# Kernel optimization log

Hardware: AMD Instinct MI355X
Metric: run time of the kernel (lower is better)

The kernel has to match this reference:

```python
import jax, jax.numpy as jnp
import numpy as np

BETA = 0.25


def setup_inputs() -> dict:
    key = jax.random.key(0)
    k1, k2, k3, k4 = jax.random.split(key, 4)
    e_dim, n_e = 512, 8192
    z = jax.random.normal(k1, (16, e_dim, 32, 32), dtype=jnp.float32)
    # nn.init.normal_(embedding.weight, std=e_dim**-0.5)
    emb_weight = jax.random.normal(k2, (n_e, e_dim), dtype=jnp.float32) * (e_dim ** -0.5)
    # torch Linear default init ~ U(-1/sqrt(in), 1/sqrt(in))
    lim = 1.0 / np.sqrt(e_dim)
    proj_w = jax.random.uniform(k3, (e_dim, e_dim), minval=-lim, maxval=lim, dtype=jnp.float32)
    proj_b = jax.random.uniform(k4, (e_dim,), minval=-lim, maxval=lim, dtype=jnp.float32)
    return {"z": z, "emb_weight": emb_weight, "proj_w": proj_w, "proj_b": proj_b}


def reference(z, emb_weight, proj_w, proj_b):
    # z: [B, C, H, W] -> [B, H, W, C]
    zc = jnp.transpose(z, (0, 2, 3, 1))
    B, H, W, C = zc.shape
    z_flat = zc.reshape(-1, C)                               # [N, C]
    # projected codebook: Linear(e_dim, e_dim) -> x @ W^T + b
    qc = emb_weight @ proj_w.T + proj_b                      # [n_e, C]
    # squared distances: ||z||^2 + ||qc||^2 - 2 z.qc
    d = (jnp.sum(z_flat ** 2, axis=1, keepdims=True)
         + jnp.sum(qc ** 2, axis=1)
         - 2.0 * jnp.einsum('nd,kd->nk', z_flat, qc))        # [N, n_e]
    idx = jnp.argmin(d, axis=1)                              # [N]
    z_q = qc[idx].reshape(zc.shape)                          # [B, H, W, C]
    # legacy=False commit loss
    commit_loss = (BETA * jnp.mean((jax.lax.stop_gradient(z_q) - zc) ** 2)
                   + jnp.mean((z_q - jax.lax.stop_gradient(zc)) ** 2))
    # straight-through
    z_q = zc + jax.lax.stop_gradient(z_q - zc)
    z_q = jnp.transpose(z_q, (0, 3, 1, 2))                   # [B, C, H, W]
    min_encoding_indices = idx.reshape(B, H, W)              # sane_index_shape=True
    return z_q, commit_loss, min_encoding_indices
```

## Files before the change

kernel.cpp:

```cpp
#include <hip/hip_runtime.h>

typedef unsigned int uint;
typedef unsigned short ushort;
typedef unsigned long long ulong64;
typedef __attribute__((ext_vector_type(8))) short short8;
typedef __attribute__((ext_vector_type(4))) float f32x4;

#define B_   16
#define C_   512
#define HW_  1024
#define N_   16384
#define K_   8192
#define EPS_ 0.25f

#define QC_OFF    0u
#define QC_SZ     (K_ * C_)
#define QN_OFF    (QC_OFF + QC_SZ)
#define QN_SZ     K_
#define ZN_OFF    (QN_OFF + QN_SZ)
#define ZN_SZ     N_
#define ZF_OFF    (ZN_OFF + ZN_SZ)
#define ZF_SZ     (N_ * C_)
#define ZH_OFF    (ZF_OFF + ZF_SZ)
#define ZH_SZ     (N_ * C_ / 2)
#define QH_OFF    (ZH_OFF + ZH_SZ)
#define QH_SZ     (K_ * C_ / 2)
#define WT_OFF    (QH_OFF + QH_SZ)
#define WT_SZ     (64 * N_ * 4)
#define IDXF_OFF  (WT_OFF + WT_SZ)
#define IDXF_SZ   N_
#define LOSS_OFF  (IDXF_OFF + IDXF_SZ)

#define OUT_ZQ    0
#define OUT_LOSS  8388608
#define OUT_IDX   8388609

__device__ __forceinline__ ushort f2bf(float f) {
    uint x = __float_as_uint(f);
    uint r = x + 0x7fffu + ((x >> 16) & 1u);
    return (ushort)(r >> 16);
}

__global__ __launch_bounds__(256) void transpose_z(const float* __restrict__ z,
                                                   float* __restrict__ zf,
                                                   ushort* __restrict__ zh) {
    __shared__ float ld[64][65];
    const int t = threadIdx.x;
    const int mt = blockIdx.x, ct = blockIdx.y, b = blockIdx.z;
    {
        const int cl = t >> 4, m4 = (t & 15) * 4;
#pragma unroll
        for (int cc = 0; cc < 4; ++cc) {
            const int c = ct * 64 + cc * 16 + cl;
            float4 v = *(const float4*)&z[((size_t)(b * 512 + c)) * 1024 + mt * 64 + m4];
            ld[cc * 16 + cl][m4 + 0] = v.x; ld[cc * 16 + cl][m4 + 1] = v.y;
            ld[cc * 16 + cl][m4 + 2] = v.z; ld[cc * 16 + cl][m4 + 3] = v.w;
        }
    }
    __syncthreads();
    {
        const int nl = t >> 4, c4 = (t & 15) * 4;
#pragma unroll
        for (int nn = 0; nn < 4; ++nn) {
            const int n_local = nn * 16 + nl;
            const size_t n = (size_t)b * 1024 + mt * 64 + n_local;
            float4 w;
            w.x = ld[c4 + 0][n_local]; w.y = ld[c4 + 1][n_local];
            w.z = ld[c4 + 2][n_local]; w.w = ld[c4 + 3][n_local];
            *(float4*)&zf[n * 512 + ct * 64 + c4] = w;
            ushort4 h; h.x = f2bf(w.x); h.y = f2bf(w.y); h.z = f2bf(w.z); h.w = f2bf(w.w);
            *(ushort4*)&zh[n * 512 + ct * 64 + c4] = h;
        }
    }
}

__global__ __launch_bounds__(256) void qc_gemm(const float* __restrict__ emb,
                                               const float* __restrict__ W,
                                               const float* __restrict__ bias,
                                               float* __restrict__ qc,
                                               ushort* __restrict__ qh) {
    __shared__ float As[16][132];
    __shared__ float Bs[16][68];
    const int t    = threadIdx.x;
    const int k0   = blockIdx.x * 128;
    const int c0   = blockIdx.y * 64;
    const int ty   = t >> 4, tx = t & 15;
    const int rowA = t >> 1;
    const int dqA  = (t & 1) * 8;
    const int rowB = t >> 2;
    const int dqB  = (t & 3) * 4;

    const float* pa = emb + (size_t)(k0 + rowA) * 512 + dqA;
    const float* pb = W   + (size_t)(c0 + rowB) * 512 + dqB;
    float4 ra0 = *(const float4*)&pa[0];
    float4 ra1 = *(const float4*)&pa[4];
    float4 rb  = *(const float4*)&pb[0];

    float acc[2][4][4] = {};
    for (int d0 = 0; d0 < 512; d0 += 16) {
        __syncthreads();
        As[dqA + 0][rowA] = ra0.x; As[dqA + 1][rowA] = ra0.y;
        As[dqA + 2][rowA] = ra0.z; As[dqA + 3][rowA] = ra0.w;
        As[dqA + 4][rowA] = ra1.x; As[dqA + 5][rowA] = ra1.y;
        As[dqA + 6][rowA] = ra1.z; As[dqA + 7][rowA] = ra1.w;
        Bs[dqB + 0][rowB] = rb.x;  Bs[dqB + 1][rowB] = rb.y;
        Bs[dqB + 2][rowB] = rb.z;  Bs[dqB + 3][rowB] = rb.w;
        if (d0 + 16 < 512) {
            ra0 = *(const float4*)&pa[d0 + 16];
            ra1 = *(const float4*)&pa[d0 + 20];
            rb  = *(const float4*)&pb[d0 + 16];
        }
        __syncthreads();
#pragma unroll
        for (int dd = 0; dd < 16; ++dd) {
            float4 a0 = *(const float4*)&As[dd][ty * 4];
            float4 a1 = *(const float4*)&As[dd][64 + ty * 4];
            float4 b0 = *(const float4*)&Bs[dd][tx * 4];
            float aa[2][4] = {{a0.x, a0.y, a0.z, a0.w}, {a1.x, a1.y, a1.z, a1.w}};
            float bb[4] = {b0.x, b0.y, b0.z, b0.w};
#pragma unroll
            for (int ih = 0; ih < 2; ++ih)
#pragma unroll
                for (int i = 0; i < 4; ++i)
#pragma unroll
                    for (int j = 0; j < 4; ++j)
                        acc[ih][i][j] += aa[ih][i] * bb[j];
        }
    }
#pragma unroll
    for (int ih = 0; ih < 2; ++ih)
#pragma unroll
        for (int i = 0; i < 4; ++i) {
            const size_t kr = (size_t)(k0 + ih * 64 + ty * 4 + i) * 512;
            const int cb = c0 + tx * 4;
            float4 v;
            v.x = acc[ih][i][0] + bias[cb + 0];
            v.y = acc[ih][i][1] + bias[cb + 1];
            v.z = acc[ih][i][2] + bias[cb + 2];
            v.w = acc[ih][i][3] + bias[cb + 3];
            *(float4*)&qc[kr + cb] = v;
            ushort4 h; h.x = f2bf(v.x); h.y = f2bf(v.y); h.z = f2bf(v.z); h.w = f2bf(v.w);
            *(ushort4*)&qh[kr + cb] = h;
        }
}

__global__ __launch_bounds__(256) void znorm_pairwise(const float* __restrict__ z,
                                                      float* __restrict__ zn) {
#pragma clang fp contract(off)
    const int n = blockIdx.x * 256 + threadIdx.x;
    const int b = n >> 10, m = n & 1023;
    const float* base = z + (size_t)b * C_ * HW_ + m;
    float s128[4];
#pragma unroll
    for (int blk = 0; blk < 4; ++blk) {
        float r[8];
#pragma unroll
        for (int j = 0; j < 8; ++j) {
            float v = base[(size_t)(blk * 128 + j) * HW_];
            r[j] = v * v;
        }
#pragma unroll 1
        for (int i = 8; i < 128; i += 8) {
#pragma unroll
            for (int j = 0; j < 8; ++j) {
                float v = base[(size_t)(blk * 128 + i + j) * HW_];
                float sq = v * v;
                r[j] = r[j] + sq;
            }
        }
        s128[blk] = ((r[0] + r[1]) + (r[2] + r[3])) + ((r[4] + r[5]) + (r[6] + r[7]));
    }
    zn[n] = (s128[0] + s128[1]) + (s128[2] + s128[3]);
}

__global__ __launch_bounds__(256) void qnorm_grouped(const float* __restrict__ qc,
                                                     float* __restrict__ qn) {
#pragma clang fp contract(off)
    const int t   = threadIdx.x;
    const int grp = t >> 3;
    const int j   = t & 7;
    const int k   = blockIdx.x * 32 + grp;
    const float* row = qc + (size_t)k * C_;
    float s[4];
#pragma unroll
    for (int blk = 0; blk < 4; ++blk) {
        float v0 = row[blk * 128 + j];
        float r  = v0 * v0;
#pragma unroll 1
        for (int i = 1; i < 16; ++i) {
            float v  = row[blk * 128 + i * 8 + j];
            float sq = v * v;
            r = r + sq;
        }
        float t1 = r  + __shfl_xor(r, 1, 64);
        float t2 = t1 + __shfl_xor(t1, 2, 64);
        float t3 = t2 + __shfl_xor(t2, 4, 64);
        s[blk] = t3;
    }
    if (j == 0) qn[k] = (s[0] + s[1]) + (s[2] + s[3]);
}

#define PH_BAR()   __builtin_amdgcn_s_barrier()
#define PH_LGKM()  asm volatile("s_waitcnt lgkmcnt(0)" ::: "memory")
#define PH_LGKM8() asm volatile("s_waitcnt lgkmcnt(8)" ::: "memory")
#define PH_VM4()   asm volatile("s_waitcnt vmcnt(4)" ::: "memory")

__device__ __forceinline__ short8 ld8(const short* p, int off) {
    return *(const short8*)(p + off);
}

__global__ __launch_bounds__(512, 2) void phaseA(const ushort* __restrict__ qh,
                                                 const ushort* __restrict__ zh,
                                                 const float* __restrict__ qn,
                                                 float* __restrict__ wtop) {
    __shared__ short lq[32768];
    __shared__ short lz[32768];
    const int t    = threadIdx.x;
    const int lane = t & 63;
    const int wv   = t >> 6;
    const int wk   = wv >> 2;
    const int wn   = wv & 3;
    const int n0   = blockIdx.x * 256;
    const int k0   = blockIdx.y * 256;

    const int l15 = lane & 15;
    const int hi8 = (lane >> 4) << 3;
    const int xr  = (l15 & 7) << 3;
    const short* pA0 = lq + wk * 8192 + l15 * 64 + ((hi8) ^ xr);
    const short* pA1 = lq + wk * 8192 + l15 * 64 + ((32 + hi8) ^ xr);
    const short* pB0 = lz + (wn >> 1) * 8192 + (wn & 1) * 4096 + l15 * 64 + ((hi8) ^ xr);
    const short* pB1 = lz + (wn >> 1) * 8192 + (wn & 1) * 4096 + l15 * 64 + ((32 + hi8) ^ xr);

    const int ch0 = t,        row0 = ch0 >> 3;
    const int ch1 = t + 512,  row1 = ch1 >> 3;
    const int ce0 = ((ch0 ^ row0) & 7) << 3;
    const int ce1 = ((ch1 ^ row1) & 7) << 3;
    const ushort* qsrc0 = qh + (size_t)(k0 + row0) * 512 + ce0;
    const ushort* qsrc1 = qh + (size_t)(k0 + row1) * 512 + ce1;
    const ushort* zsrc0 = zh + (size_t)(n0 + row0) * 512 + ce0;
    const ushort* zsrc1 = zh + (size_t)(n0 + row1) * 512 + ce1;
    short* qdst0 = lq + ch0 * 8;
    short* qdst1 = lq + ch1 * 8;
    short* zdst0 = lz + ch0 * 8;
    short* zdst1 = lz + ch1 * 8;

    auto stage_half = [&](int b, int h, int chunk) {
        const int co = chunk * 64;
        if (h < 2) {
            __builtin_amdgcn_global_load_lds(
                (const __attribute__((address_space(1))) uint*)(qsrc0 + h * 65536 + co),
                (__attribute__((address_space(3))) uint*)(qdst0 + (b * 2 + h) * 8192), 16, 0, 0);
            __builtin_amdgcn_global_load_lds(
                (const __attribute__((address_space(1))) uint*)(qsrc1 + h * 65536 + co),
                (__attribute__((address_space(3))) uint*)(qdst1 + (b * 2 + h) * 8192), 16, 0, 0);
        } else {
            __builtin_amdgcn_global_load_lds(
                (const __attribute__((address_space(1))) uint*)(zsrc0 + (h - 2) * 65536 + co),
                (__attribute__((address_space(3))) uint*)(zdst0 + (b * 2 + (h - 2)) * 8192), 16, 0, 0);
            __builtin_amdgcn_global_load_lds(
                (const __attribute__((address_space(1))) uint*)(zsrc1 + (h - 2) * 65536 + co),
                (__attribute__((address_space(3))) uint*)(zdst1 + (b * 2 + (h - 2)) * 8192), 16, 0, 0);
        }
    };

    f32x4 acc[8][4];
#pragma unroll
    for (int i = 0; i < 8; ++i)
#pragma unroll
        for (int j = 0; j < 4; ++j) acc[i][j] = (f32x4){0.f, 0.f, 0.f, 0.f};

    stage_half(0, 0, 0); stage_half(0, 1, 0); stage_half(0, 2, 0); stage_half(0, 3, 0);
    stage_half(1, 0, 1); stage_half(1, 1, 1);
    PH_VM4();
    PH_BAR();

    short8 a0[2][4], a1[2][4], b0[2][2], b1[2][2];

#pragma unroll 1
    for (int I = 0; I < 4; ++I) {
        const int tE = 2 * I;
        const int tO = 2 * I + 1;

#pragma unroll
        for (int i = 0; i < 4; ++i) {
            a0[0][i] = ld8(pA0, i * 1024);        a0[1][i] = ld8(pA1, i * 1024);
            a1[0][i] = ld8(pA0, 4096 + i * 1024); a1[1][i] = ld8(pA1, 4096 + i * 1024);
        }
#pragma unroll
        for (int jj = 0; jj < 2; ++jj) { b0[0][jj] = ld8(pB0, jj * 1024); b0[1][jj] = ld8(pB1, jj * 1024); }
        stage_half(1, 2, (tO) & 7); stage_half(1, 3, (tO) & 7);
        PH_LGKM8();
        PH_BAR(); PH_LGKM();
        __builtin_amdgcn_s_setprio(1);
#pragma unroll
        for (int kk = 0; kk < 2; ++kk)
#pragma unroll
            for (int i = 0; i < 4; ++i)
#pragma unroll
                for (int jj = 0; jj < 2; ++jj) {
                    acc[i][jj]     = __builtin_amdgcn_mfma_f32_16x16x32_bf16(a0[kk][i], b0[kk][jj], acc[i][jj], 0, 0, 0);
                    acc[4 + i][jj] = __builtin_amdgcn_mfma_f32_16x16x32_bf16(a1[kk][i], b0[kk][jj], acc[4 + i][jj], 0, 0, 0);
                }
        __builtin_amdgcn_s_setprio(0);
        PH_BAR();
#pragma unroll
        for (int jj = 0; jj < 2; ++jj) { b1[0][jj] = ld8(pB0, 2048 + jj * 1024); b1[1][jj] = ld8(pB1, 2048 + jj * 1024); }
        stage_half(0, 0, (tE + 2) & 7); stage_half(0, 1, (tE + 2) & 7);
        PH_BAR(); PH_LGKM();
        __builtin_amdgcn_s_setprio(1);
#pragma unroll
        for (int kk = 0; kk < 2; ++kk)
#pragma unroll
            for (int i = 0; i < 4; ++i)
#pragma unroll
                for (int jj = 0; jj < 2; ++jj) {
                    acc[i][2 + jj]     = __builtin_amdgcn_mfma_f32_16x16x32_bf16(a0[kk][i], b1[kk][jj], acc[i][2 + jj], 0, 0, 0);
                    acc[4 + i][2 + jj] = __builtin_amdgcn_mfma_f32_16x16x32_bf16(a1[kk][i], b1[kk][jj], acc[4 + i][2 + jj], 0, 0, 0);
                }
        __builtin_amdgcn_s_setprio(0);
        PH_VM4();
        PH_BAR();

#pragma unroll
        for (int i = 0; i < 4; ++i) {
            a0[0][i] = ld8(pA0, 16384 + i * 1024);        a0[1][i] = ld8(pA1, 16384 + i * 1024);
            a1[0][i] = ld8(pA0, 16384 + 4096 + i * 1024); a1[1][i] = ld8(pA1, 16384 + 4096 + i * 1024);
        }
#pragma unroll
        for (int jj = 0; jj < 2; ++jj) { b0[0][jj] = ld8(pB0, 16384 + jj * 1024); b0[1][jj] = ld8(pB1, 16384 + jj * 1024); }
        stage_half(0, 2, (tO + 1) & 7); stage_half(0, 3, (tO + 1) & 7);
        PH_LGKM8();
        PH_BAR(); PH_LGKM();
        __builtin_amdgcn_s_setprio(1);
#pragma unroll
        for (int kk = 0; kk < 2; ++kk)
#pragma unroll
            for (int i = 0; i < 4; ++i)
#pragma unroll
                for (int jj = 0; jj < 2; ++jj) {
                    acc[i][jj]     = __builtin_amdgcn_mfma_f32_16x16x32_bf16(a0[kk][i], b0[kk][jj], acc[i][jj], 0, 0, 0);
                    acc[4 + i][jj] = __builtin_amdgcn_mfma_f32_16x16x32_bf16(a1[kk][i], b0[kk][jj], acc[4 + i][jj], 0, 0, 0);
                }
        __builtin_amdgcn_s_setprio(0);
        PH_BAR();
#pragma unroll
        for (int jj = 0; jj < 2; ++jj) { b1[0][jj] = ld8(pB0, 16384 + 2048 + jj * 1024); b1[1][jj] = ld8(pB1, 16384 + 2048 + jj * 1024); }
        stage_half(1, 0, (tO + 2) & 7); stage_half(1, 1, (tO + 2) & 7);
        PH_BAR(); PH_LGKM();
        __builtin_amdgcn_s_setprio(1);
#pragma unroll
        for (int kk = 0; kk < 2; ++kk)
#pragma unroll
            for (int i = 0; i < 4; ++i)
#pragma unroll
                for (int jj = 0; jj < 2; ++jj) {
                    acc[i][2 + jj]     = __builtin_amdgcn_mfma_f32_16x16x32_bf16(a0[kk][i], b1[kk][jj], acc[i][2 + jj], 0, 0, 0);
                    acc[4 + i][2 + jj] = __builtin_amdgcn_mfma_f32_16x16x32_bf16(a1[kk][i], b1[kk][jj], acc[4 + i][2 + jj], 0, 0, 0);
                }
        __builtin_amdgcn_s_setprio(0);
        PH_VM4();
        PH_BAR();
    }

    const int q4 = (lane >> 4) * 4;
    float v1[4], v2[4];
    int   k1[4], k2[4];
#pragma unroll
    for (int in = 0; in < 4; ++in) { v1[in] = 1e30f; v2[in] = 1e30f; k1[in] = 0; k2[in] = 0; }

#pragma unroll
    for (int ik = 0; ik < 8; ++ik) {
        float qv[4];
#pragma unroll
        for (int r = 0; r < 4; ++r)
            qv[r] = qn[k0 + wk * 128 + ik * 16 + q4 + r];
#pragma unroll
        for (int in = 0; in < 4; ++in) {
#pragma unroll
            for (int r = 0; r < 4; ++r) {
                const float val = qv[r] - 2.0f * acc[ik][in][r];
                const int   kg  = k0 + wk * 128 + ik * 16 + q4 + r;
                if (val < v1[in]) { v2[in] = v1[in]; k2[in] = k1[in]; v1[in] = val; k1[in] = kg; }
                else if (val < v2[in]) { v2[in] = val; k2[in] = kg; }
            }
        }
    }
#pragma unroll
    for (int m = 16; m <= 32; m <<= 1) {
#pragma unroll
        for (int in = 0; in < 4; ++in) {
            const float ov1 = __shfl_xor(v1[in], m, 64);
            const int   ok1 = __shfl_xor(k1[in], m, 64);
            const float ov2 = __shfl_xor(v2[in], m, 64);
            const int   ok2 = __shfl_xor(k2[in], m, 64);
            float nv1, nv2; int nk1, nk2;
            if (ov1 < v1[in]) {
                nv1 = ov1; nk1 = ok1;
                if (v1[in] < ov2) { nv2 = v1[in]; nk2 = k1[in]; } else { nv2 = ov2; nk2 = ok2; }
            } else {
                nv1 = v1[in]; nk1 = k1[in];
                if (ov1 < v2[in]) { nv2 = ov1; nk2 = ok1; } else { nv2 = v2[in]; nk2 = k2[in]; }
            }
            v1[in] = nv1; k1[in] = nk1; v2[in] = nv2; k2[in] = nk2;
        }
    }
    if ((lane >> 4) == 0) {
        const int w = blockIdx.y * 2 + wk;
#pragma unroll
        for (int in = 0; in < 4; ++in) {
            const int n = n0 + wn * 64 + in * 16 + (lane & 15);
            float4 o; o.x = v1[in]; o.y = __int_as_float(k1[in]);
            o.z = v2[in]; o.w = __int_as_float(k2[in]);
            *(float4*)&wtop[((size_t)n * 64 + w) * 4] = o;
        }
    }
}

__global__ __launch_bounds__(256) void phaseBC(const float* __restrict__ zf,
                                               const float* __restrict__ qc,
                                               const float* __restrict__ zn,
                                               const float* __restrict__ qn,
                                               const float* __restrict__ wtop,
                                               int* __restrict__ idxf,
                                               float* __restrict__ out_idx,
                                               float* __restrict__ loss_acc) {
    __shared__ float zr[4][512];
    __shared__ float ql[4][2][512];
    __shared__ int   clist[4][128];
    const int wv   = threadIdx.x >> 6;
    const int lane = threadIdx.x & 63;
    const int r    = blockIdx.x * 4 + wv;
    if (blockIdx.x == 0 && threadIdx.x == 0) loss_acc[0] = 0.f;

    float4 e = *(const float4*)&wtop[((size_t)r * 64 + lane) * 4];
    float rmin = e.x;
#pragma unroll
    for (int m = 1; m <= 32; m <<= 1) rmin = fminf(rmin, __shfl_xor(rmin, m, 64));
    const float thr = rmin + EPS_;
    const bool h1 = (e.x <= thr), h2 = (e.z <= thr);
    const ulong64 m1 = __ballot(h1);
    const ulong64 m2 = __ballot(h2);
    const int c1  = __popcll(m1);
    const int cnt = c1 + __popcll(m2);

    if (cnt == 1) {
        if (h1) { const int k = __float_as_int(e.y); idxf[r] = k; out_idx[r] = (float)k; }
        else if (h2) { const int k = __float_as_int(e.w); idxf[r] = k; out_idx[r] = (float)k; }
        return;
    }

    const ulong64 below = (lane == 63) ? ~0ull >> 1 : ((1ull << lane) - 1);
    if (h1) clist[wv][__popcll(m1 & below)] = __float_as_int(e.y);
    if (h2) clist[wv][c1 + __popcll(m2 & below)] = __float_as_int(e.w);

    *(float4*)&zr[wv][lane * 8]     = *(const float4*)&zf[(size_t)r * 512 + lane * 8];
    *(float4*)&zr[wv][lane * 8 + 4] = *(const float4*)&zf[(size_t)r * 512 + lane * 8 + 4];
    asm volatile("s_waitcnt lgkmcnt(0)" ::: "memory");

    const int g  = lane >> 5;
    const int cl = (lane & 31) * 16;
    const int steps = (cnt + 1) >> 1;
    const float znr = zn[r];

    auto cand_of = [&](int s) {
        const int ci = 2 * s + g;
        return clist[wv][ci < cnt ? ci : 0];
    };

    int k_cur = cand_of(0);
    const float* q0 = qc + (size_t)k_cur * 512 + cl;
    float4 p0 = *(const float4*)&q0[0];
    float4 p1 = *(const float4*)&q0[4];
    float4 p2 = *(const float4*)&q0[8];
    float4 p3 = *(const float4*)&q0[12];

    float bd = 1e30f;
    int   bi = 0x7fffffff;

    for (int s = 0; s < steps; ++s) {
        *(float4*)&ql[wv][g][cl + 0]  = p0;
        *(float4*)&ql[wv][g][cl + 4]  = p1;
        *(float4*)&ql[wv][g][cl + 8]  = p2;
        *(float4*)&ql[wv][g][cl + 12] = p3;

        int k_next = 0;
        if (s + 1 < steps) {
            k_next = cand_of(s + 1);
            const float* qn_ = qc + (size_t)k_next * 512 + cl;
            p0 = *(const float4*)&qn_[0];
            p1 = *(const float4*)&qn_[4];
            p2 = *(const float4*)&qn_[8];
            p3 = *(const float4*)&qn_[12];
        }

        float acc = 0.f;
#pragma unroll 16
        for (int c = 0; c < 512; c += 4) {
            float4 zv = *(const float4*)&zr[wv][c];
            float4 qv = *(const float4*)&ql[wv][g][c];
            acc = fmaf(zv.x, qv.x, acc);
            acc = fmaf(zv.y, qv.y, acc);
            acc = fmaf(zv.z, qv.z, acc);
            acc = fmaf(zv.w, qv.w, acc);
        }
        const float T = znr + qn[k_cur];
        const float d = T - 2.0f * acc;
        const bool valid = (2 * s + g) < cnt;
        if (valid && (d < bd || (d == bd && k_cur < bi))) { bd = d; bi = k_cur; }
        k_cur = k_next;
    }

    const float od = __shfl_xor(bd, 32, 64);
    const int   oi = __shfl_xor(bi, 32, 64);
    if (od < bd || (od == bd && oi < bi)) { bd = od; bi = oi; }

    if (lane == 0) { idxf[r] = bi; out_idx[r] = (float)bi; }
}

__global__ __launch_bounds__(256) void gather_out(const float* __restrict__ z,
                                                  const float* __restrict__ qc,
                                                  const int* __restrict__ idxf,
                                                  float* __restrict__ zq_out,
                                                  float* __restrict__ loss_acc) {
    __shared__ int   idxs[64];
    __shared__ float zqs[64][65];
    __shared__ float wsum[4];
    const int t  = threadIdx.x;
    const int mc = blockIdx.x;
    const int cc = blockIdx.y;
    const int bz = blockIdx.z;

    if (t < 64) idxs[t] = idxf[bz * 1024 + mc * 64 + t];
    __syncthreads();
    {
        const int row  = t >> 2;
        const int coff = (t & 3) * 16;
        const float* src = qc + (size_t)idxs[row] * 512 + cc * 64 + coff;
#pragma unroll
        for (int v = 0; v < 4; ++v) {
            float4 q = *(const float4*)&src[v * 4];
            zqs[row][coff + v * 4 + 0] = q.x;
            zqs[row][coff + v * 4 + 1] = q.y;
            zqs[row][coff + v * 4 + 2] = q.z;
            zqs[row][coff + v * 4 + 3] = q.w;
        }
    }
    __syncthreads();

    float ls = 0.f;
    {
        const int c_local = t >> 2;
        const int mg      = (t & 3) * 16;
        const size_t gbase = ((size_t)(bz * 512 + cc * 64 + c_local)) * 1024 + mc * 64 + mg;
#pragma unroll
        for (int v = 0; v < 4; ++v) {
            const int m = mg + v * 4;
            float4 w;
            w.x = zqs[m + 0][c_local];
            w.y = zqs[m + 1][c_local];
            w.z = zqs[m + 2][c_local];
            w.w = zqs[m + 3][c_local];
            float4 zv = *(const float4*)&z[gbase + v * 4];
            float dx = w.x - zv.x, dy = w.y - zv.y, dz = w.z - zv.z, dw = w.w - zv.w;
            ls += dx * dx + dy * dy + dz * dz + dw * dw;
            *(float4*)&zq_out[gbase + v * 4] = w;
        }
    }
#pragma unroll
    for (int m = 32; m; m >>= 1) ls += __shfl_xor(ls, m, 64);
    const int lane = t & 63, wvv = t >> 6;
    if (lane == 0) wsum[wvv] = ls;
    __syncthreads();
    if (t == 0) atomicAdd(loss_acc, wsum[0] + wsum[1] + wsum[2] + wsum[3]);
}

__global__ void finalize(const float* __restrict__ loss_acc,
                         float* __restrict__ out_loss) {
    out_loss[0] = 1.25f * loss_acc[0] / 8388608.0f;
}

extern "C" void kernel_launch(void* const* d_in, const int* in_sizes, int n_in,
                              void* d_out, int out_size, void* d_ws, size_t ws_size,
                              hipStream_t stream) {
    const float* z    = (const float*)d_in[0];
    const float* emb  = (const float*)d_in[1];
    const float* W    = (const float*)d_in[2];
    const float* bias = (const float*)d_in[3];
    float* ws = (float*)d_ws;

    float*  qc       = ws + QC_OFF;
    float*  qn       = ws + QN_OFF;
    float*  zn       = ws + ZN_OFF;
    float*  zf       = ws + ZF_OFF;
    ushort* zh       = (ushort*)(ws + ZH_OFF);
    ushort* qh       = (ushort*)(ws + QH_OFF);
    float*  wtop     = ws + WT_OFF;
    int*    idxf     = (int*)(ws + IDXF_OFF);
    float*  loss_acc = ws + LOSS_OFF;
    float*  out      = (float*)d_out;

    transpose_z<<<dim3(16, 8, 16), 256, 0, stream>>>(z, zf, zh);
    qc_gemm<<<dim3(K_ / 128, C_ / 64), 256, 0, stream>>>(emb, W, bias, qc, qh);
    qnorm_grouped<<<K_ / 32, 256, 0, stream>>>(qc, qn);
    znorm_pairwise<<<N_ / 256, 256, 0, stream>>>(z, zn);
    phaseA<<<dim3(N_ / 256, K_ / 256), 512, 0, stream>>>(qh, zh, qn, wtop);
    phaseBC<<<N_ / 4, 256, 0, stream>>>(zf, qc, zn, qn, wtop, idxf, out + OUT_IDX, loss_acc);
    gather_out<<<dim3(16, 8, B_), 256, 0, stream>>>(z, qc, idxf, out + OUT_ZQ, loss_acc);
    finalize<<<1, 1, 0, stream>>>(loss_acc, out + OUT_LOSS);
}
```

Measured before the change: 387.7 us.

## Load z operand directly from global into registers, drop z LDS staging

The phaseA distance GEMM no longer stages the z (bf16) tile through shared memory. Each wave loads its B fragments straight from global memory into registers, one K-chunk ahead, while the codebook tile still goes through LDS with global_load_lds double buffering. This halves LDS usage and removes some barriers and LDS reads. In exchange, each wave issues uncoalesced-ish 16-byte global loads that are repeated across the waves sharing an n slice, and the loop now depends on global latency being hidden with a vmcnt wait.

Measured after the change: 449.3 us. 15.9% more time.

```diff
diff --git a/kernel.cpp b/kernel.cpp
--- a/kernel.cpp
+++ b/kernel.cpp
@@ -202,8 +202,8 @@
 
 #define PH_BAR()   __builtin_amdgcn_s_barrier()
 #define PH_LGKM()  asm volatile("s_waitcnt lgkmcnt(0)" ::: "memory")
-#define PH_LGKM8() asm volatile("s_waitcnt lgkmcnt(8)" ::: "memory")
 #define PH_VM4()   asm volatile("s_waitcnt vmcnt(4)" ::: "memory")
+#define PH_VM8()   asm volatile("s_waitcnt vmcnt(8)" ::: "memory")
 
 __device__ __forceinline__ short8 ld8(const short* p, int off) {
     return *(const short8*)(p + off);
@@ -214,7 +214,6 @@
                                                  const float* __restrict__ qn,
                                                  float* __restrict__ wtop) {
     __shared__ short lq[32768];
-    __shared__ short lz[32768];
     const int t    = threadIdx.x;
     const int lane = t & 63;
     const int wv   = t >> 6;
@@ -228,8 +227,6 @@
     const int xr  = (l15 & 7) << 3;
     const short* pA0 = lq + wk * 8192 + l15 * 64 + ((hi8) ^ xr);
     const short* pA1 = lq + wk * 8192 + l15 * 64 + ((32 + hi8) ^ xr);
-    const short* pB0 = lz + (wn >> 1) * 8192 + (wn & 1) * 4096 + l15 * 64 + ((hi8) ^ xr);
-    const short* pB1 = lz + (wn >> 1) * 8192 + (wn & 1) * 4096 + l15 * 64 + ((32 + hi8) ^ xr);
 
     const int ch0 = t,        row0 = ch0 >> 3;
     const int ch1 = t + 512,  row1 = ch1 >> 3;
@@ -237,60 +234,59 @@
     const int ce1 = ((ch1 ^ row1) & 7) << 3;
     const ushort* qsrc0 = qh + (size_t)(k0 + row0) * 512 + ce0;
     const ushort* qsrc1 = qh + (size_t)(k0 + row1) * 512 + ce1;
-    const ushort* zsrc0 = zh + (size_t)(n0 + row0) * 512 + ce0;
-    const ushort* zsrc1 = zh + (size_t)(n0 + row1) * 512 + ce1;
     short* qdst0 = lq + ch0 * 8;
     short* qdst1 = lq + ch1 * 8;
-    short* zdst0 = lz + ch0 * 8;
-    short* zdst1 = lz + ch1 * 8;
-
-    auto stage_half = [&](int b, int h, int chunk) {
+
+    auto stageA = [&](int b, int chunk) {
         const int co = chunk * 64;
-        if (h < 2) {
+#pragma unroll
+        for (int h = 0; h < 2; ++h) {
             __builtin_amdgcn_global_load_lds(
                 (const __attribute__((address_space(1))) uint*)(qsrc0 + h * 65536 + co),
                 (__attribute__((address_space(3))) uint*)(qdst0 + (b * 2 + h) * 8192), 16, 0, 0);
             __builtin_amdgcn_global_load_lds(
                 (const __attribute__((address_space(1))) uint*)(qsrc1 + h * 65536 + co),
                 (__attribute__((address_space(3))) uint*)(qdst1 + (b * 2 + h) * 8192), 16, 0, 0);
-        } else {
-            __builtin_amdgcn_global_load_lds(
-                (const __attribute__((address_space(1))) uint*)(zsrc0 + (h - 2) * 65536 + co),
-                (__attribute__((address_space(3))) uint*)(zdst0 + (b * 2 + (h - 2)) * 8192), 16, 0, 0);
-            __builtin_amdgcn_global_load_lds(
-                (const __attribute__((address_space(1))) uint*)(zsrc1 + (h - 2) * 65536 + co),
-                (__attribute__((address_space(3))) uint*)(zdst1 + (b * 2 + (h - 2)) * 8192), 16, 0, 0);
         }
     };
 
+    const ushort* zb = zh + (size_t)(n0 + wn * 64 + l15) * 512 + hi8;
+    short8 b01[2][2], b23[2][2];
+
     f32x4 acc[8][4];
 #pragma unroll
     for (int i = 0; i < 8; ++i)
 #pragma unroll
         for (int j = 0; j < 4; ++j) acc[i][j] = (f32x4){0.f, 0.f, 0.f, 0.f};
 
-    stage_half(0, 0, 0); stage_half(0, 1, 0); stage_half(0, 2, 0); stage_half(0, 3, 0);
-    stage_half(1, 0, 1); stage_half(1, 1, 1);
+    stageA(0, 0);
+#pragma unroll
+    for (int kk = 0; kk < 2; ++kk)
+#pragma unroll
+        for (int jj = 0; jj < 2; ++jj)
+            b01[kk][jj] = *(const short8*)(zb + (size_t)jj * 8192 + kk * 32);
+#pragma unroll
+    for (int kk = 0; kk < 2; ++kk)
+#pragma unroll
+        for (int jj = 0; jj < 2; ++jj)
+            b23[kk][jj] = *(const short8*)(zb + (size_t)(2 + jj) * 8192 + kk * 32);
+    stageA(1, 1);
     PH_VM4();
     PH_BAR();
 
-    short8 a0[2][4], a1[2][4], b0[2][2], b1[2][2];
+    short8 a0[2][4], a1[2][4];
 
 #pragma unroll 1
-    for (int I = 0; I < 4; ++I) {
-        const int tE = 2 * I;
-        const int tO = 2 * I + 1;
+    for (int tt = 0; tt < 8; ++tt) {
+        const int bo = (tt & 1) * 16384;
 
 #pragma unroll
         for (int i = 0; i < 4; ++i) {
-            a0[0][i] = ld8(pA0, i * 1024);        a0[1][i] = ld8(pA1, i * 1024);
-            a1[0][i] = ld8(pA0, 4096 + i * 1024); a1[1][i] = ld8(pA1, 4096 + i * 1024);
-        }
-#pragma unroll
-        for (int jj = 0; jj < 2; ++jj) { b0[0][jj] = ld8(pB0, jj * 1024); b0[1][jj] = ld8(pB1, jj * 1024); }
-        stage_half(1, 2, (tO) & 7); stage_half(1, 3, (tO) & 7);
-        PH_LGKM8();
-        PH_BAR(); PH_LGKM();
+            a0[0][i] = ld8(pA0, bo + i * 1024);        a0[1][i] = ld8(pA1, bo + i * 1024);
+            a1[0][i] = ld8(pA0, bo + 4096 + i * 1024); a1[1][i] = ld8(pA1, bo + 4096 + i * 1024);
+        }
+        PH_LGKM();
+        PH_VM4();
         __builtin_amdgcn_s_setprio(1);
 #pragma unroll
         for (int kk = 0; kk < 2; ++kk)
@@ -298,15 +294,22 @@
             for (int i = 0; i < 4; ++i)
 #pragma unroll
                 for (int jj = 0; jj < 2; ++jj) {
-                    acc[i][jj]     = __builtin_amdgcn_mfma_f32_16x16x32_bf16(a0[kk][i], b0[kk][jj], acc[i][jj], 0, 0, 0);
-                    acc[4 + i][jj] = __builtin_amdgcn_mfma_f32_16x16x32_bf16(a1[kk][i], b0[kk][jj], acc[4 + i][jj], 0, 0, 0);
+                    acc[i][jj]     = __builtin_amdgcn_mfma_f32_16x16x32_bf16(a0[kk][i], b01[kk][jj], acc[i][jj], 0, 0, 0);
+                    acc[4 + i][jj] = __builtin_amdgcn_mfma_f32_16x16x32_bf16(a1[kk][i], b01[kk][jj], acc[4 + i][jj], 0, 0, 0);
                 }
         __builtin_amdgcn_s_setprio(0);
         PH_BAR();
-#pragma unroll
-        for (int jj = 0; jj < 2; ++jj) { b1[0][jj] = ld8(pB0, 2048 + jj * 1024); b1[1][jj] = ld8(pB1, 2048 + jj * 1024); }
-        stage_half(0, 0, (tE + 2) & 7); stage_half(0, 1, (tE + 2) & 7);
-        PH_BAR(); PH_LGKM();
+
+        stageA(tt & 1, (tt + 2) & 7);
+        {
+            const int c0n = ((tt + 1) & 7) * 64;
+#pragma unroll
+            for (int kk = 0; kk < 2; ++kk)
+#pragma unroll
+                for (int jj = 0; jj < 2; ++jj)
+                    b01[kk][jj] = *(const short8*)(zb + (size_t)jj * 8192 + c0n + kk * 32);
+        }
+        PH_VM8();
         __builtin_amdgcn_s_setprio(1);
 #pragma unroll
         for (int kk = 0; kk < 2; ++kk)
@@ -314,51 +317,18 @@
             for (int i = 0; i < 4; ++i)
 #pragma unroll
                 for (int jj = 0; jj < 2; ++jj) {
-                    acc[i][2 + jj]     = __builtin_amdgcn_mfma_f32_16x16x32_bf16(a0[kk][i], b1[kk][jj], acc[i][2 + jj], 0, 0, 0);
-                    acc[4 + i][2 + jj] = __builtin_amdgcn_mfma_f32_16x16x32_bf16(a1[kk][i], b1[kk][jj], acc[4 + i][2 + jj], 0, 0, 0);
+                    acc[i][2 + jj]     = __builtin_amdgcn_mfma_f32_16x16x32_bf16(a0[kk][i], b23[kk][jj], acc[i][2 + jj], 0, 0, 0);
+                    acc[4 + i][2 + jj] = __builtin_amdgcn_mfma_f32_16x16x32_bf16(a1[kk][i], b23[kk][jj], acc[4 + i][2 + jj], 0, 0, 0);
                 }
         __builtin_amdgcn_s_setprio(0);
-        PH_VM4();
-        PH_BAR();
-
-#pragma unroll
-        for (int i = 0; i < 4; ++i) {
-            a0[0][i] = ld8(pA0, 16384 + i * 1024);        a0[1][i] = ld8(pA1, 16384 + i * 1024);
-            a1[0][i] = ld8(pA0, 16384 + 4096 + i * 1024); a1[1][i] = ld8(pA1, 16384 + 4096 + i * 1024);
-        }
-#pragma unroll
-        for (int jj = 0; jj < 2; ++jj) { b0[0][jj] = ld8(pB0, 16384 + jj * 1024); b0[1][jj] = ld8(pB1, 16384 + jj * 1024); }
-        stage_half(0, 2, (tO + 1) & 7); stage_half(0, 3, (tO + 1) & 7);
-        PH_LGKM8();
-        PH_BAR(); PH_LGKM();
-        __builtin_amdgcn_s_setprio(1);
-#pragma unroll
-        for (int kk = 0; kk < 2; ++kk)
-#pragma unroll
-            for (int i = 0; i < 4; ++i)
-#pragma unroll
-                for (int jj = 0; jj < 2; ++jj) {
-                    acc[i][jj]     = __builtin_amdgcn_mfma_f32_16x16x32_bf16(a0[kk][i], b0[kk][jj], acc[i][jj], 0, 0, 0);
-                    acc[4 + i][jj] = __builtin_amdgcn_mfma_f32_16x16x32_bf16(a1[kk][i], b0[kk][jj], acc[4 + i][jj], 0, 0, 0);
-                }
-        __builtin_amdgcn_s_setprio(0);
-        PH_BAR();
-#pragma unroll
-        for (int jj = 0; jj < 2; ++jj) { b1[0][jj] = ld8(pB0, 16384 + 2048 + jj * 1024); b1[1][jj] = ld8(pB1, 16384 + 2048 + jj * 1024); }
-        stage_half(1, 0, (tO + 2) & 7); stage_half(1, 1, (tO + 2) & 7);
-        PH_BAR(); PH_LGKM();
-        __builtin_amdgcn_s_setprio(1);
-#pragma unroll
-        for (int kk = 0; kk < 2; ++kk)
-#pragma unroll
-            for (int i = 0; i < 4; ++i)
-#pragma unroll
-                for (int jj = 0; jj < 2; ++jj) {
-                    acc[i][2 + jj]     = __builtin_amdgcn_mfma_f32_16x16x32_bf16(a0[kk][i], b1[kk][jj], acc[i][2 + jj], 0, 0, 0);
-                    acc[4 + i][2 + jj] = __builtin_amdgcn_mfma_f32_16x16x32_bf16(a1[kk][i], b1[kk][jj], acc[4 + i][2 + jj], 0, 0, 0);
-                }
-        __builtin_amdgcn_s_setprio(0);
-        PH_VM4();
+        {
+            const int c0n = ((tt + 1) & 7) * 64;
+#pragma unroll
+            for (int kk = 0; kk < 2; ++kk)
+#pragma unroll
+                for (int jj = 0; jj < 2; ++jj)
+                    b23[kk][jj] = *(const short8*)(zb + (size_t)(2 + jj) * 8192 + c0n + kk * 32);
+        }
         PH_BAR();
     }
 
```

## Make phaseA blocks loop over eight K tiles and widen phaseBC candidate parallelism

Applied to the files above, without the earlier changes.

phaseA now launches 4 blocks along K instead of 32, and each block walks eight consecutive 256-wide codebook tiles. The global-to-LDS prefetch runs on across tile boundaries, so the next tile's first chunk loads while the current tile finishes its epilogue, and the per-block prologue cost is paid fewer times. phaseBC now has four lane groups each score one candidate per step instead of two groups, which cuts the number of serial steps per row at the cost of more LDS and registers. The risks are fewer blocks in phaseA (256 in total), which may leave compute units idle, and lower occupancy in phaseBC.

Measured after the change: 391.5 us. Within noise of the previous version (+1.0%).

```diff
diff --git a/kernel.cpp b/kernel.cpp
--- a/kernel.cpp
+++ b/kernel.cpp
@@ -204,6 +204,7 @@
 #define PH_LGKM()  asm volatile("s_waitcnt lgkmcnt(0)" ::: "memory")
 #define PH_LGKM8() asm volatile("s_waitcnt lgkmcnt(8)" ::: "memory")
 #define PH_VM4()   asm volatile("s_waitcnt vmcnt(4)" ::: "memory")
+#define PH_VM0()   asm volatile("s_waitcnt vmcnt(0)" ::: "memory")
 
 __device__ __forceinline__ short8 ld8(const short* p, int off) {
     return *(const short8*)(p + off);
@@ -221,7 +222,6 @@
     const int wk   = wv >> 2;
     const int wn   = wv & 3;
     const int n0   = blockIdx.x * 256;
-    const int k0   = blockIdx.y * 256;
 
     const int l15 = lane & 15;
     const int hi8 = (lane >> 4) << 3;
@@ -235,8 +235,8 @@
     const int ch1 = t + 512,  row1 = ch1 >> 3;
     const int ce0 = ((ch0 ^ row0) & 7) << 3;
     const int ce1 = ((ch1 ^ row1) & 7) << 3;
-    const ushort* qsrc0 = qh + (size_t)(k0 + row0) * 512 + ce0;
-    const ushort* qsrc1 = qh + (size_t)(k0 + row1) * 512 + ce1;
+    const ushort* qsrc0 = qh + (size_t)row0 * 512 + ce0;
+    const ushort* qsrc1 = qh + (size_t)row1 * 512 + ce1;
     const ushort* zsrc0 = zh + (size_t)(n0 + row0) * 512 + ce0;
     const ushort* zsrc1 = zh + (size_t)(n0 + row1) * 512 + ce1;
     short* qdst0 = lq + ch0 * 8;
@@ -244,9 +244,11 @@
     short* zdst0 = lz + ch0 * 8;
     short* zdst1 = lz + ch1 * 8;
 
-    auto stage_half = [&](int b, int h, int chunk) {
-        const int co = chunk * 64;
+    size_t koff = (size_t)blockIdx.y * 8 * 131072;
+
+    auto stage_half = [&](int b, int h, int ci) {
         if (h < 2) {
+            const size_t co = koff + (size_t)((ci & 7) * 64 + (ci >> 3) * 131072);
             __builtin_amdgcn_global_load_lds(
                 (const __attribute__((address_space(1))) uint*)(qsrc0 + h * 65536 + co),
                 (__attribute__((address_space(3))) uint*)(qdst0 + (b * 2 + h) * 8192), 16, 0, 0);
@@ -254,6 +256,7 @@
                 (const __attribute__((address_space(1))) uint*)(qsrc1 + h * 65536 + co),
                 (__attribute__((address_space(3))) uint*)(qdst1 + (b * 2 + h) * 8192), 16, 0, 0);
         } else {
+            const int co = (ci & 7) * 64;
             __builtin_amdgcn_global_load_lds(
                 (const __attribute__((address_space(1))) uint*)(zsrc0 + (h - 2) * 65536 + co),
                 (__attribute__((address_space(3))) uint*)(zdst0 + (b * 2 + (h - 2)) * 8192), 16, 0, 0);
@@ -264,154 +267,161 @@
     };
 
     f32x4 acc[8][4];
-#pragma unroll
-    for (int i = 0; i < 8; ++i)
-#pragma unroll
-        for (int j = 0; j < 4; ++j) acc[i][j] = (f32x4){0.f, 0.f, 0.f, 0.f};
+    short8 a0[2][4], a1[2][4], b0[2][2], b1[2][2];
 
     stage_half(0, 0, 0); stage_half(0, 1, 0); stage_half(0, 2, 0); stage_half(0, 3, 0);
     stage_half(1, 0, 1); stage_half(1, 1, 1);
     PH_VM4();
     PH_BAR();
 
-    short8 a0[2][4], a1[2][4], b0[2][2], b1[2][2];
-
 #pragma unroll 1
-    for (int I = 0; I < 4; ++I) {
-        const int tE = 2 * I;
-        const int tO = 2 * I + 1;
-
-#pragma unroll
-        for (int i = 0; i < 4; ++i) {
-            a0[0][i] = ld8(pA0, i * 1024);        a0[1][i] = ld8(pA1, i * 1024);
-            a1[0][i] = ld8(pA0, 4096 + i * 1024); a1[1][i] = ld8(pA1, 4096 + i * 1024);
-        }
-#pragma unroll
-        for (int jj = 0; jj < 2; ++jj) { b0[0][jj] = ld8(pB0, jj * 1024); b0[1][jj] = ld8(pB1, jj * 1024); }
-        stage_half(1, 2, (tO) & 7); stage_half(1, 3, (tO) & 7);
-        PH_LGKM8();
-        PH_BAR(); PH_LGKM();
-        __builtin_amdgcn_s_setprio(1);
-#pragma unroll
-        for (int kk = 0; kk < 2; ++kk)
-#pragma unroll
-            for (int i = 0; i < 4; ++i)
-#pragma unroll
-                for (int jj = 0; jj < 2; ++jj) {
-                    acc[i][jj]     = __builtin_amdgcn_mfma_f32_16x16x32_bf16(a0[kk][i], b0[kk][jj], acc[i][jj], 0, 0, 0);
-                    acc[4 + i][jj] = __builtin_amdgcn_mfma_f32_16x16x32_bf16(a1[kk][i], b0[kk][jj], acc[4 + i][jj], 0, 0, 0);
+    for (int yp = 0; yp < 8; ++yp) {
+        koff = (size_t)(blockIdx.y * 8 + yp) * 131072;
+        const int k0e = (blockIdx.y * 8 + yp) * 256;
+
+#pragma unroll
+        for (int i = 0; i < 8; ++i)
+#pragma unroll
+            for (int j = 0; j < 4; ++j) acc[i][j] = (f32x4){0.f, 0.f, 0.f, 0.f};
+
+#pragma unroll 1
+        for (int I = 0; I < 4; ++I) {
+            const int t1 = 2 * I + 1;
+            const int t2 = 2 * I + 2;
+            const int t3 = 2 * I + 3;
+
+#pragma unroll
+            for (int i = 0; i < 4; ++i) {
+                a0[0][i] = ld8(pA0, i * 1024);        a0[1][i] = ld8(pA1, i * 1024);
+                a1[0][i] = ld8(pA0, 4096 + i * 1024); a1[1][i] = ld8(pA1, 4096 + i * 1024);
+            }
+#pragma unroll
+            for (int jj = 0; jj < 2; ++jj) { b0[0][jj] = ld8(pB0, jj * 1024); b0[1][jj] = ld8(pB1, jj * 1024); }
+            stage_half(1, 2, t1); stage_half(1, 3, t1);
+            PH_LGKM8();
+            PH_BAR(); PH_LGKM();
+            __builtin_amdgcn_s_setprio(1);
+#pragma unroll
+            for (int kk = 0; kk < 2; ++kk)
+#pragma unroll
+                for (int i = 0; i < 4; ++i)
+#pragma unroll
+                    for (int jj = 0; jj < 2; ++jj) {
+                        acc[i][jj]     = __builtin_amdgcn_mfma_f32_16x16x32_bf16(a0[kk][i], b0[kk][jj], acc[i][jj], 0, 0, 0);
+                        acc[4 + i][jj] = __builtin_amdgcn_mfma_f32_16x16x32_bf16(a1[kk][i], b0[kk][jj], acc[4 + i][jj], 0, 0, 0);
+                    }
+            __builtin_amdgcn_s_setprio(0);
+            PH_BAR();
+#pragma unroll
+            for (int jj = 0; jj < 2; ++jj) { b1[0][jj] = ld8(pB0, 2048 + jj * 1024); b1[1][jj] = ld8(pB1, 2048 + jj * 1024); }
+            stage_half(0, 0, t2); stage_half(0, 1, t2);
+            PH_BAR(); PH_LGKM();
+            __builtin_amdgcn_s_setprio(1);
+#pragma unroll
+            for (int kk = 0; kk < 2; ++kk)
+#pragma unroll
+                for (int i = 0; i < 4; ++i)
+#pragma unroll
+                    for (int jj = 0; jj < 2; ++jj) {
+                        acc[i][2 + jj]     = __builtin_amdgcn_mfma_f32_16x16x32_bf16(a0[kk][i], b1[kk][jj], acc[i][2 + jj], 0, 0, 0);
+                        acc[4 + i][2 + jj] = __builtin_amdgcn_mfma_f32_16x16x32_bf16(a1[kk][i], b1[kk][jj], acc[4 + i][2 + jj], 0, 0, 0);
+                    }
+            __builtin_amdgcn_s_setprio(0);
+            PH_VM4();
+            PH_BAR();
+
+#pragma unroll
+            for (int i = 0; i < 4; ++i) {
+                a0[0][i] = ld8(pA0, 16384 + i * 1024);        a0[1][i] = ld8(pA1, 16384 + i * 1024);
+                a1[0][i] = ld8(pA0, 16384 + 4096 + i * 1024); a1[1][i] = ld8(pA1, 16384 + 4096 + i * 1024);
+            }
+#pragma unroll
+            for (int jj = 0; jj < 2; ++jj) { b0[0][jj] = ld8(pB0, 16384 + jj * 1024); b0[1][jj] = ld8(pB1, 16384 + jj * 1024); }
+            stage_half(0, 2, t2); stage_half(0, 3, t2);
+            PH_LGKM8();
+            PH_BAR(); PH_LGKM();
+            __builtin_amdgcn_s_setprio(1);
+#pragma unroll
+            for (int kk = 0; kk < 2; ++kk)
+#pragma unroll
+                for (int i = 0; i < 4; ++i)
+#pragma unroll
+                    for (int jj = 0; jj < 2; ++jj) {
+                        acc[i][jj]     = __builtin_amdgcn_mfma_f32_16x16x32_bf16(a0[kk][i], b0[kk][jj], acc[i][jj], 0, 0, 0);
+                        acc[4 + i][jj] = __builtin_amdgcn_mfma_f32_16x16x32_bf16(a1[kk][i], b0[kk][jj], acc[4 + i][jj], 0, 0, 0);
+                    }
+            __builtin_amdgcn_s_setprio(0);
+            PH_BAR();
+#pragma unroll
+            for (int jj = 0; jj < 2; ++jj) { b1[0][jj] = ld8(pB0, 16384 + 2048 + jj * 1024); b1[1][jj] = ld8(pB1, 16384 + 2048 + jj * 1024); }
+            stage_half(1, 0, t3); stage_half(1, 1, t3);
+            PH_BAR(); PH_LGKM();
+            __builtin_amdgcn_s_setprio(1);
+#pragma unroll
+            for (int kk = 0; kk < 2; ++kk)
+#pragma unroll
+                for (int i = 0; i < 4; ++i)
+#pragma unroll
+                    for (int jj = 0; jj < 2; ++jj) {
+                        acc[i][2 + jj]     = __builtin_amdgcn_mfma_f32_16x16x32_bf16(a0[kk][i], b1[kk][jj], acc[i][2 + jj], 0, 0, 0);
+                        acc[4 + i][2 + jj] = __builtin_amdgcn_mfma_f32_16x16x32_bf16(a1[kk][i], b1[kk][jj], acc[4 + i][2 + jj], 0, 0, 0);
+                    }
+            __builtin_amdgcn_s_setprio(0);
+            if (I == 3) { PH_VM0(); } else { PH_VM4(); }
+            PH_BAR();
+        }
+
+        const int q4 = (lane >> 4) * 4;
+        float v1[4], v2[4];
+        int   k1[4], k2[4];
+#pragma unroll
+        for (int in = 0; in < 4; ++in) { v1[in] = 1e30f; v2[in] = 1e30f; k1[in] = 0; k2[in] = 0; }
+
+#pragma unroll
+        for (int ik = 0; ik < 8; ++ik) {
+            float qv[4];
+#pragma unroll
+            for (int r = 0; r < 4; ++r)
+                qv[r] = qn[k0e + wk * 128 + ik * 16 + q4 + r];
+#pragma unroll
+            for (int in = 0; in < 4; ++in) {
+#pragma unroll
+                for (int r = 0; r < 4; ++r) {
+                    const float val = qv[r] - 2.0f * acc[ik][in][r];
+                    const int   kg  = k0e + wk * 128 + ik * 16 + q4 + r;
+                    if (val < v1[in]) { v2[in] = v1[in]; k2[in] = k1[in]; v1[in] = val; k1[in] = kg; }
+                    else if (val < v2[in]) { v2[in] = val; k2[in] = kg; }
                 }
-        __builtin_amdgcn_s_setprio(0);
-        PH_BAR();
-#pragma unroll
-        for (int jj = 0; jj < 2; ++jj) { b1[0][jj] = ld8(pB0, 2048 + jj * 1024); b1[1][jj] = ld8(pB1, 2048 + jj * 1024); }
-        stage_half(0, 0, (tE + 2) & 7); stage_half(0, 1, (tE + 2) & 7);
-        PH_BAR(); PH_LGKM();
-        __builtin_amdgcn_s_setprio(1);
-#pragma unroll
-        for (int kk = 0; kk < 2; ++kk)
-#pragma unroll
-            for (int i = 0; i < 4; ++i)
-#pragma unroll
-                for (int jj = 0; jj < 2; ++jj) {
-                    acc[i][2 + jj]     = __builtin_amdgcn_mfma_f32_16x16x32_bf16(a0[kk][i], b1[kk][jj], acc[i][2 + jj], 0, 0, 0);
-                    acc[4 + i][2 + jj] = __builtin_amdgcn_mfma_f32_16x16x32_bf16(a1[kk][i], b1[kk][jj], acc[4 + i][2 + jj], 0, 0, 0);
+            }
+        }
+#pragma unroll
+        for (int m = 16; m <= 32; m <<= 1) {
+#pragma unroll
+            for (int in = 0; in < 4; ++in) {
+                const float ov1 = __shfl_xor(v1[in], m, 64);
+                const int   ok1 = __shfl_xor(k1[in], m, 64);
+                const float ov2 = __shfl_xor(v2[in], m, 64);
+                const int   ok2 = __shfl_xor(k2[in], m, 64);
+                float nv1, nv2; int nk1, nk2;
+                if (ov1 < v1[in]) {
+                    nv1 = ov1; nk1 = ok1;
+                    if (v1[in] < ov2) { nv2 = v1[in]; nk2 = k1[in]; } else { nv2 = ov2; nk2 = ok2; }
+                } else {
+                    nv1 = v1[in]; nk1 = k1[in];
+                    if (ov1 < v2[in]) { nv2 = ov1; nk2 = ok1; } else { nv2 = v2[in]; nk2 = k2[in]; }
                 }
-        __builtin_amdgcn_s_setprio(0);
-        PH_VM4();
-        PH_BAR();
-
-#pragma unroll
-        for (int i = 0; i < 4; ++i) {
-            a0[0][i] = ld8(pA0, 16384 + i * 1024);        a0[1][i] = ld8(pA1, 16384 + i * 1024);
-            a1[0][i] = ld8(pA0, 16384 + 4096 + i * 1024); a1[1][i] = ld8(pA1, 16384 + 4096 + i * 1024);
-        }
-#pragma unroll
-        for (int jj = 0; jj < 2; ++jj) { b0[0][jj] = ld8(pB0, 16384 + jj * 1024); b0[1][jj] = ld8(pB1, 16384 + jj * 1024); }
-        stage_half(0, 2, (tO + 1) & 7); stage_half(0, 3, (tO + 1) & 7);
-        PH_LGKM8();
-        PH_BAR(); PH_LGKM();
-        __builtin_amdgcn_s_setprio(1);
-#pragma unroll
-        for (int kk = 0; kk < 2; ++kk)
-#pragma unroll
-            for (int i = 0; i < 4; ++i)
-#pragma unroll
-                for (int jj = 0; jj < 2; ++jj) {
-                    acc[i][jj]     = __builtin_amdgcn_mfma_f32_16x16x32_bf16(a0[kk][i], b0[kk][jj], acc[i][jj], 0, 0, 0);
-                    acc[4 + i][jj] = __builtin_amdgcn_mfma_f32_16x16x32_bf16(a1[kk][i], b0[kk][jj], acc[4 + i][jj], 0, 0, 0);
-                }
-        __builtin_amdgcn_s_setprio(0);
-        PH_BAR();
-#pragma unroll
-        for (int jj = 0; jj < 2; ++jj) { b1[0][jj] = ld8(pB0, 16384 + 2048 + jj * 1024); b1[1][jj] = ld8(pB1, 16384 + 2048 + jj * 1024); }
-        stage_half(1, 0, (tO + 2) & 7); stage_half(1, 1, (tO + 2) & 7);
-        PH_BAR(); PH_LGKM();
-        __builtin_amdgcn_s_setprio(1);
-#pragma unroll
-        for (int kk = 0; kk < 2; ++kk)
-#pragma unroll
-            for (int i = 0; i < 4; ++i)
-#pragma unroll
-                for (int jj = 0; jj < 2; ++jj) {
-                    acc[i][2 + jj]     = __builtin_amdgcn_mfma_f32_16x16x32_bf16(a0[kk][i], b1[kk][jj], acc[i][2 + jj], 0, 0, 0);
-                    acc[4 + i][2 + jj] = __builtin_amdgcn_mfma_f32_16x16x32_bf16(a1[kk][i], b1[kk][jj], acc[4 + i][2 + jj], 0, 0, 0);
-                }
-        __builtin_amdgcn_s_setprio(0);
-        PH_VM4();
-        PH_BAR();
-    }
-
-    const int q4 = (lane >> 4) * 4;
-    float v1[4], v2[4];
-    int   k1[4], k2[4];
-#pragma unroll
-    for (int in = 0; in < 4; ++in) { v1[in] = 1e30f; v2[in] = 1e30f; k1[in] = 0; k2[in] = 0; }
-
-#pragma unroll
-    for (int ik = 0; ik < 8; ++ik) {
-        float qv[4];
-#pragma unroll
-        for (int r = 0; r < 4; ++r)
-            qv[r] = qn[k0 + wk * 128 + ik * 16 + q4 + r];
-#pragma unroll
-        for (int in = 0; in < 4; ++in) {
-#pragma unroll
-            for (int r = 0; r < 4; ++r) {
-                const float val = qv[r] - 2.0f * acc[ik][in][r];
-                const int   kg  = k0 + wk * 128 + ik * 16 + q4 + r;
-                if (val < v1[in]) { v2[in] = v1[in]; k2[in] = k1[in]; v1[in] = val; k1[in] = kg; }
-                else if (val < v2[in]) { v2[in] = val; k2[in] = kg; }
+                v1[in] = nv1; k1[in] = nk1; v2[in] = nv2; k2[in] = nk2;
             }
         }
-    }
-#pragma unroll
-    for (int m = 16; m <= 32; m <<= 1) {
-#pragma unroll
-        for (int in = 0; in < 4; ++in) {
-            const float ov1 = __shfl_xor(v1[in], m, 64);
-            const int   ok1 = __shfl_xor(k1[in], m, 64);
-            const float ov2 = __shfl_xor(v2[in], m, 64);
-            const int   ok2 = __shfl_xor(k2[in], m, 64);
-            float nv1, nv2; int nk1, nk2;
-            if (ov1 < v1[in]) {
-                nv1 = ov1; nk1 = ok1;
-                if (v1[in] < ov2) { nv2 = v1[in]; nk2 = k1[in]; } else { nv2 = ov2; nk2 = ok2; }
-            } else {
-                nv1 = v1[in]; nk1 = k1[in];
-                if (ov1 < v2[in]) { nv2 = ov1; nk2 = ok1; } else { nv2 = v2[in]; nk2 = k2[in]; }
+        if ((lane >> 4) == 0) {
+            const int w = (blockIdx.y * 8 + yp) * 2 + wk;
+#pragma unroll
+            for (int in = 0; in < 4; ++in) {
+                const int n = n0 + wn * 64 + in * 16 + (lane & 15);
+                float4 o; o.x = v1[in]; o.y = __int_as_float(k1[in]);
+                o.z = v2[in]; o.w = __int_as_float(k2[in]);
+                *(float4*)&wtop[((size_t)n * 64 + w) * 4] = o;
             }
-            v1[in] = nv1; k1[in] = nk1; v2[in] = nv2; k2[in] = nk2;
-        }
-    }
-    if ((lane >> 4) == 0) {
-        const int w = blockIdx.y * 2 + wk;
-#pragma unroll
-        for (int in = 0; in < 4; ++in) {
-            const int n = n0 + wn * 64 + in * 16 + (lane & 15);
-            float4 o; o.x = v1[in]; o.y = __int_as_float(k1[in]);
-            o.z = v2[in]; o.w = __int_as_float(k2[in]);
-            *(float4*)&wtop[((size_t)n * 64 + w) * 4] = o;
         }
     }
 }
@@ -425,7 +435,7 @@
                                                float* __restrict__ out_idx,
                                                float* __restrict__ loss_acc) {
     __shared__ float zr[4][512];
-    __shared__ float ql[4][2][512];
+    __shared__ float ql[4][4][512];
     __shared__ int   clist[4][128];
     const int wv   = threadIdx.x >> 6;
     const int lane = threadIdx.x & 63;
@@ -457,13 +467,13 @@
     *(float4*)&zr[wv][lane * 8 + 4] = *(const float4*)&zf[(size_t)r * 512 + lane * 8 + 4];
     asm volatile("s_waitcnt lgkmcnt(0)" ::: "memory");
 
-    const int g  = lane >> 5;
-    const int cl = (lane & 31) * 16;
-    const int steps = (cnt + 1) >> 1;
+    const int g  = lane >> 4;
+    const int cl = (lane & 15) * 32;
+    const int steps = (cnt + 3) >> 2;
     const float znr = zn[r];
 
     auto cand_of = [&](int s) {
-        const int ci = 2 * s + g;
+        const int ci = 4 * s + g;
         return clist[wv][ci < cnt ? ci : 0];
     };
 
@@ -473,6 +483,10 @@
     float4 p1 = *(const float4*)&q0[4];
     float4 p2 = *(const float4*)&q0[8];
     float4 p3 = *(const float4*)&q0[12];
+    float4 p4 = *(const float4*)&q0[16];
+    float4 p5 = *(const float4*)&q0[20];
+    float4 p6 = *(const float4*)&q0[24];
+    float4 p7 = *(const float4*)&q0[28];
 
     float bd = 1e30f;
     int   bi = 0x7fffffff;
@@ -482,6 +496,10 @@
         *(float4*)&ql[wv][g][cl + 4]  = p1;
         *(float4*)&ql[wv][g][cl + 8]  = p2;
         *(float4*)&ql[wv][g][cl + 12] = p3;
+        *(float4*)&ql[wv][g][cl + 16] = p4;
+        *(float4*)&ql[wv][g][cl + 20] = p5;
+        *(float4*)&ql[wv][g][cl + 24] = p6;
+        *(float4*)&ql[wv][g][cl + 28] = p7;
 
         int k_next = 0;
         if (s + 1 < steps) {
@@ -491,6 +509,10 @@
             p1 = *(const float4*)&qn_[4];
             p2 = *(const float4*)&qn_[8];
             p3 = *(const float4*)&qn_[12];
+            p4 = *(const float4*)&qn_[16];
+            p5 = *(const float4*)&qn_[20];
+            p6 = *(const float4*)&qn_[24];
+            p7 = *(const float4*)&qn_[28];
         }
 
         float acc = 0.f;
@@ -505,14 +527,21 @@
         }
         const float T = znr + qn[k_cur];
         const float d = T - 2.0f * acc;
-        const bool valid = (2 * s + g) < cnt;
+        const bool valid = (4 * s + g) < cnt;
         if (valid && (d < bd || (d == bd && k_cur < bi))) { bd = d; bi = k_cur; }
         k_cur = k_next;
     }
 
-    const float od = __shfl_xor(bd, 32, 64);
-    const int   oi = __shfl_xor(bi, 32, 64);
-    if (od < bd || (od == bd && oi < bi)) { bd = od; bi = oi; }
+    {
+        const float od = __shfl_xor(bd, 16, 64);
+        const int   oi = __shfl_xor(bi, 16, 64);
+        if (od < bd || (od == bd && oi < bi)) { bd = od; bi = oi; }
+    }
+    {
+        const float od = __shfl_xor(bd, 32, 64);
+        const int   oi = __shfl_xor(bi, 32, 64);
+        if (od < bd || (od == bd && oi < bi)) { bd = od; bi = oi; }
+    }
 
     if (lane == 0) { idxf[r] = bi; out_idx[r] = (float)bi; }
 }
@@ -603,7 +632,7 @@
     qc_gemm<<<dim3(K_ / 128, C_ / 64), 256, 0, stream>>>(emb, W, bias, qc, qh);
     qnorm_grouped<<<K_ / 32, 256, 0, stream>>>(qc, qn);
     znorm_pairwise<<<N_ / 256, 256, 0, stream>>>(z, zn);
-    phaseA<<<dim3(N_ / 256, K_ / 256), 512, 0, stream>>>(qh, zh, qn, wtop);
+    phaseA<<<dim3(N_ / 256, 4), 512, 0, stream>>>(qh, zh, qn, wtop);
     phaseBC<<<N_ / 4, 256, 0, stream>>>(zf, qc, zn, qn, wtop, idxf, out + OUT_IDX, loss_acc);
     gather_out<<<dim3(16, 8, B_), 256, 0, stream>>>(z, qc, idxf, out + OUT_ZQ, loss_acc);
     finalize<<<1, 1, 0, stream>>>(loss_acc, out + OUT_LOSS);
```
